# Kernel optimization log

Hardware: AMD Instinct MI355X
Metric: run time of the kernel (lower is better)

Reference implementation:

```python
import jax, jax.numpy as jnp
import numpy as np

HEADS = 4
DIM_HEAD = 32
SCALE = 10.0
EPS = 1e-12

def l2norm_axis1(t):
    # Faithful to source: default axis=1 -> normalize over the SEQUENCE axis of [B,N,h,d]
    denom = jnp.clip(jnp.linalg.norm(t, ord=2, axis=1, keepdims=True), EPS)
    return t / denom

def setup_inputs() -> dict:
    key = jax.random.key(0)
    k1, k2, k3 = jax.random.split(key, 3)
    B, N, C = 4, 4096, 128
    dim = HEADS * DIM_HEAD  # 128
    x = jax.random.normal(k1, (B, N, C), dtype=jnp.float32)
    W_qkv = jax.random.normal(k2, (C, 3 * dim), dtype=jnp.float32) * (1.0 / np.sqrt(C))
    W_out = jax.random.normal(k3, (dim, C), dtype=jnp.float32) * (1.0 / np.sqrt(dim))
    b_out = jnp.zeros((C,), dtype=jnp.float32)
    return {"x": x, "W_qkv": W_qkv, "W_out": W_out, "b_out": b_out}

def reference(x, W_qkv, W_out, b_out):
    B, N, C = x.shape
    # 1x1 conv == per-token linear
    qkv = jnp.einsum('bnc,ce->bne', x, W_qkv)  # [B,N,3*dim]
    q, k, v = jnp.split(qkv, 3, axis=-1)
    # [B,N,h,d]
    q = q.reshape(B, N, HEADS, DIM_HEAD)
    k = k.reshape(B, N, HEADS, DIM_HEAD)
    v = v.reshape(B, N, HEADS, DIM_HEAD)
    q = l2norm_axis1(q)
    k = l2norm_axis1(k)
    sim = jnp.einsum('bihd,bjhd->bhij', q, k) * SCALE  # [B,h,N,N]
    attn = jax.nn.softmax(sim, axis=-1)
    out = jnp.einsum('bhij,bjhd->bhid', attn, v)  # [B,h,N,d]
    out = out.transpose(0, 2, 1, 3).reshape(B, N, HEADS * DIM_HEAD)  # [B,N,dim]
    return jnp.einsum('bne,ec->bnc', out, W_out) + b_out
```

## Files before the change

### kernel.cpp

```cpp
#include <hip/hip_runtime.h>

typedef short s16x8 __attribute__((ext_vector_type(8)));
typedef short s16x4 __attribute__((ext_vector_type(4)));
typedef float f32x4 __attribute__((ext_vector_type(4)));
typedef float f4 __attribute__((ext_vector_type(4)));
typedef unsigned short u16x4 __attribute__((ext_vector_type(4)));

#define CEXP 14.426950408889634074f

__device__ __forceinline__ unsigned short f2bf(float f) {
    union { float f; unsigned int i; } v; v.f = f;
    unsigned int x = v.i;
    return (unsigned short)((x + 0x7fffu + ((x >> 16) & 1u)) >> 16);
}
__device__ __forceinline__ float bf2f(unsigned short u) {
    union { unsigned int i; float f; } v; v.i = ((unsigned int)u) << 16; return v.f;
}

__device__ __forceinline__ f32x4 mfma16x16x16_bf16(s16x4 a, s16x4 b, f32x4 c) {
#if __has_builtin(__builtin_amdgcn_mfma_f32_16x16x16bf16_1k)
    return __builtin_amdgcn_mfma_f32_16x16x16bf16_1k(a, b, c, 0, 0, 0);
#else
    f32x4 d = c;
    asm("v_mfma_f32_16x16x16_bf16 %0, %1, %2, %0" : "+v"(d) : "v"(a), "v"(b));
    return d;
#endif
}

__device__ __forceinline__ s16x4 pk_bf16x4(float p0, float p1, float p2, float p3) {
#if __has_builtin(__builtin_amdgcn_cvt_pk_bf16_f32)
    typedef __bf16 bf16x2 __attribute__((ext_vector_type(2)));
    union { struct { bf16x2 a, b; } h; s16x4 s; } r;
    r.h.a = __builtin_amdgcn_cvt_pk_bf16_f32(p0, p1);
    r.h.b = __builtin_amdgcn_cvt_pk_bf16_f32(p2, p3);
    return r.s;
#else
    unsigned u0 = __float_as_uint(p0) + 0x8000u;
    unsigned u1 = __float_as_uint(p1) + 0x8000u;
    unsigned u2 = __float_as_uint(p2) + 0x8000u;
    unsigned u3 = __float_as_uint(p3) + 0x8000u;
    union { uint2 u; s16x4 s; } pb;
    pb.u.x = __builtin_amdgcn_perm(u1, u0, 0x07060302u);
    pb.u.y = __builtin_amdgcn_perm(u3, u2, 0x07060302u);
    return pb.s;
#endif
}

__device__ __forceinline__ u16x4 pk4(f4 v) {
    u16x4 r = { f2bf(v[0]), f2bf(v[1]), f2bf(v[2]), f2bf(v[3]) };
    return r;
}

__global__ __launch_bounds__(256) void k_prep(
    const float* __restrict__ Wqkv, const float* __restrict__ Wout,
    unsigned short* __restrict__ Wt, unsigned short* __restrict__ WoT,
    float* __restrict__ sumsqp)
{
    const int blk = blockIdx.x, tid = threadIdx.x;
    if (blk < 192) {
        int e = blk * 256 + tid;
        int n = e >> 7, k = e & 127;
        Wt[e] = f2bf(Wqkv[k * 384 + n]);
    } else if (blk < 256) {
        int e = (blk - 192) * 256 + tid;
        int n = e >> 7, k = e & 127;
        WoT[e] = f2bf(Wout[k * 128 + n]);
    } else {
        sumsqp[(blk - 256) * 256 + tid] = 0.f;
    }
}

__global__ __launch_bounds__(256, 4) void k_qkv(
    const float* __restrict__ x, const unsigned short* __restrict__ Wt,
    unsigned short* __restrict__ Qb, unsigned short* __restrict__ Kb,
    unsigned short* __restrict__ Vt, float* __restrict__ sumsqp)
{
    __shared__ float red[4][64];
    const int tid = threadIdx.x;
    const int wl = tid >> 6, lane = tid & 63;
    const int qd = lane >> 4, nn = lane & 15;
    const int n0 = blockIdx.y * 64;
    const int tw0 = blockIdx.x * 64 + wl * 16;

    const float* apf = x + (size_t)(tw0 + nn) * 128 + qd * 8;
    const unsigned short* bp = Wt + (size_t)(n0 + nn) * 128 + qd * 8;
    s16x8 af[4], bfr[16];
#pragma unroll
    for (int ks = 0; ks < 4; ++ks) {
        f4 a0 = *(const f4*)(apf + ks * 32);
        f4 a1 = *(const f4*)(apf + ks * 32 + 4);
        union { struct { s16x4 lo, hi; } h; s16x8 v; } u;
        u.h.lo = pk_bf16x4(a0[0], a0[1], a0[2], a0[3]);
        u.h.hi = pk_bf16x4(a1[0], a1[1], a1[2], a1[3]);
        af[ks] = u.v;
    }
#pragma unroll
    for (int nb = 0; nb < 4; ++nb)
#pragma unroll
        for (int ks = 0; ks < 4; ++ks)
            bfr[nb * 4 + ks] = *(const s16x8*)(bp + (size_t)nb * 2048 + ks * 32);

    f32x4 acc[4];
#pragma unroll
    for (int nb = 0; nb < 4; ++nb) acc[nb] = (f32x4){0.f, 0.f, 0.f, 0.f};

    const int cb = n0 >> 7;
    const int b = tw0 >> 12;
    const int tl0 = tw0 & 4095;

    if (cb < 2) {
#pragma unroll
        for (int ks = 0; ks < 4; ++ks)
#pragma unroll
            for (int nb = 0; nb < 4; ++nb)
                acc[nb] = __builtin_amdgcn_mfma_f32_16x16x32_bf16(bfr[nb * 4 + ks], af[ks], acc[nb], 0, 0, 0);
        unsigned short* dst = (cb == 0) ? Qb : Kb;
        const int tok = tl0 + nn;
#pragma unroll
        for (int nb = 0; nb < 4; ++nb) {
            const int dim = (n0 & 127) + nb * 16 + qd * 4;
            const int h = dim >> 5, d0 = dim & 31;
            *(u16x4*)&dst[(size_t)((b * 4 + h) * 4096 + tok) * 32 + d0] = pk4(acc[nb]);
            f32x4 ss;
#pragma unroll
            for (int r = 0; r < 4; ++r) ss[r] = acc[nb][r] * acc[nb][r];
#pragma unroll
            for (int m = 1; m < 16; m <<= 1) {
#pragma unroll
                for (int r = 0; r < 4; ++r) ss[r] += __shfl_xor(ss[r], m);
            }
            if (nn == 0)
                *(f4*)&red[wl][nb * 16 + qd * 4] = ss;
        }
        __syncthreads();
        if (tid < 64) {
            float s = red[0][tid] + red[1][tid] + red[2][tid] + red[3][tid];
            const int g = (cb << 9) + (b << 7) + (n0 & 127) + tid;
            atomicAdd(&sumsqp[((blockIdx.x & 7) << 10) + g], s);
        }
    } else {
#pragma unroll
        for (int ks = 0; ks < 4; ++ks)
#pragma unroll
            for (int nb = 0; nb < 4; ++nb)
                acc[nb] = __builtin_amdgcn_mfma_f32_16x16x32_bf16(af[ks], bfr[nb * 4 + ks], acc[nb], 0, 0, 0);
#pragma unroll
        for (int nb = 0; nb < 4; ++nb) {
            const int dim = (n0 & 127) + nb * 16 + nn;
            const int h = dim >> 5, d = dim & 31;
            *(u16x4*)&Vt[(size_t)((b * 4 + h) * 32 + d) * 4096 + tl0 + qd * 4] = pk4(acc[nb]);
        }
    }
}

__global__ __launch_bounds__(512, 2) void k_attn(
    const unsigned short* __restrict__ Qb, const unsigned short* __restrict__ Kb,
    const unsigned short* __restrict__ Vt, const float* __restrict__ sumsqp,
    unsigned short* __restrict__ Ogb)
{
    __shared__ char smem[32768];
    const int tid  = threadIdx.x;
    const int wv   = tid >> 6, lane = tid & 63;
    const int wl   = wv & 3, half = wv >> 2;
    const int qd   = lane >> 4, nn = lane & 15;
    const int bh   = blockIdx.x;
    const int ib   = blockIdx.y * 128 + wl * 32;
    const unsigned short* Qbh = Qb + (size_t)bh * 4096 * 32;
    const unsigned short* Kbh = Kb + (size_t)bh * 4096 * 32;
    const unsigned short* Vbh = Vt + (size_t)bh * 32 * 4096;

    float rj[8];
    {
        const int gq = bh * 32 + qd * 8;
#pragma unroll
        for (int j = 0; j < 8; ++j) {
            float sq = 0.f, sk = 0.f;
#pragma unroll
            for (int c = 0; c < 8; ++c) {
                sq += sumsqp[c * 1024 + gq + j];
                sk += sumsqp[c * 1024 + 512 + gq + j];
            }
            rj[j] = fminf(__builtin_amdgcn_rsqf(sq), 1e12f)
                  * fminf(__builtin_amdgcn_rsqf(sk), 1e12f) * CEXP;
        }
    }

    s16x8 q0r = *(const s16x8*)(Qbh + (ib + nn) * 32 + qd * 8);
    s16x8 q1r = *(const s16x8*)(Qbh + (ib + 16 + nn) * 32 + qd * 8);
    s16x8 qf0, qf1;
#pragma unroll
    for (int j = 0; j < 8; ++j) {
        qf0[j] = (short)f2bf(bf2f((unsigned short)q0r[j]) * rj[j]);
        qf1[j] = (short)f2bf(bf2f((unsigned short)q1r[j]) * rj[j]);
    }

    f32x4 o00 = {0.f,0.f,0.f,0.f}, o01 = {0.f,0.f,0.f,0.f};
    f32x4 o10 = {0.f,0.f,0.f,0.f}, o11 = {0.f,0.f,0.f,0.f};
    const f32x4 zro = {0.f,0.f,0.f,0.f};
    float lpa = 0.f, lpb = 0.f;

    const int KB0 = half * 8192;
    const int VB0 = 16384 + half * 8192;
    const int jb0 = half * 2048;

    const unsigned short* ksrc = Kbh + (size_t)(jb0 + wl * 16 + nn) * 32 + qd * 8;
    const unsigned short* vsrc = Vbh + (size_t)(nn + 16 * (wl >> 1)) * 4096
                               + jb0 + ((wl & 1) * 2 + (qd >> 1)) * 16 + (qd & 1) * 8;
    char* kdst = smem + KB0 + wl * 1024 + lane * 16;
    char* vdst = smem + VB0 + wl * 1024 + lane * 16;

    {
        uint4 gk = *(const uint4*)ksrc;
        uint4 gv = *(const uint4*)vsrc;
        ksrc += 2048; vsrc += 64;
        *(uint4*)kdst = gk;
        *(uint4*)vdst = gv;
    }

    const int vro = (qd >> 1) * 256 + nn * 16 + (qd & 1) * 8;

    for (int jt = 0; jt < 32; ++jt) {
        uint4 ngk = *(const uint4*)ksrc;
        uint4 ngv = *(const uint4*)vsrc;
        ksrc += 2048; vsrc += 64;

        __syncthreads();
        const char* kcur = smem + KB0 + (jt & 1) * 4096;
        const char* vcur = smem + VB0 + (jt & 1) * 4096;
#pragma unroll
        for (int js = 0; js < 4; ++js) {
            s16x8 kf = *(const s16x8*)(kcur + js * 1024 + lane * 16);
            f32x4 sa = __builtin_amdgcn_mfma_f32_16x16x32_bf16(kf, qf0, zro, 0, 0, 0);
            f32x4 sb = __builtin_amdgcn_mfma_f32_16x16x32_bf16(kf, qf1, zro, 0, 0, 0);
            float a0 = __builtin_amdgcn_exp2f(sa[0]);
            float a1 = __builtin_amdgcn_exp2f(sa[1]);
            float a2 = __builtin_amdgcn_exp2f(sa[2]);
            float a3 = __builtin_amdgcn_exp2f(sa[3]);
            float b0 = __builtin_amdgcn_exp2f(sb[0]);
            float b1 = __builtin_amdgcn_exp2f(sb[1]);
            float b2 = __builtin_amdgcn_exp2f(sb[2]);
            float b3 = __builtin_amdgcn_exp2f(sb[3]);
            lpa += (a0 + a1) + (a2 + a3);
            lpb += (b0 + b1) + (b2 + b3);
            s16x4 pa = pk_bf16x4(a0, a1, a2, a3);
            s16x4 pb = pk_bf16x4(b0, b1, b2, b3);
            s16x4 va = *(const s16x4*)(vcur + js * 512 + vro);
            s16x4 vb = *(const s16x4*)(vcur + 2048 + js * 512 + vro);
            o00 = mfma16x16x16_bf16(va, pa, o00);
            o01 = mfma16x16x16_bf16(vb, pa, o01);
            o10 = mfma16x16x16_bf16(va, pb, o10);
            o11 = mfma16x16x16_bf16(vb, pb, o11);
        }
        const int nxt4k = ((jt + 1) & 1) * 4096;
        *(uint4*)(kdst + nxt4k) = ngk;
        *(uint4*)(vdst + nxt4k) = ngv;
    }

    lpa += __shfl_xor(lpa, 16);
    lpa += __shfl_xor(lpa, 32);
    lpb += __shfl_xor(lpb, 16);
    lpb += __shfl_xor(lpb, 32);
    __syncthreads();
    float* Ob = (float*)smem;
    float* Lb = (float*)(smem + 16384);
    if (half) {
        float* d0 = Ob + ((wl * 2 + 0) * 64 + lane) * 8;
        *(f4*)d0 = o00; *(f4*)(d0 + 4) = o01;
        float* d1 = Ob + ((wl * 2 + 1) * 64 + lane) * 8;
        *(f4*)d1 = o10; *(f4*)(d1 + 4) = o11;
        Lb[(wl * 2 + 0) * 64 + lane] = lpa;
        Lb[(wl * 2 + 1) * 64 + lane] = lpb;
    }
    __syncthreads();
    if (!half) {
        const int bb = bh >> 2, hh = bh & 3;
        float* s0 = Ob + ((wl * 2 + 0) * 64 + lane) * 8;
        float rla = 1.f / (lpa + Lb[(wl * 2 + 0) * 64 + lane]);
        f4 m00 = (o00 + *(const f4*)s0) * rla;
        f4 m01 = (o01 + *(const f4*)(s0 + 4)) * rla;
        float* s1 = Ob + ((wl * 2 + 1) * 64 + lane) * 8;
        float rlb = 1.f / (lpb + Lb[(wl * 2 + 1) * 64 + lane]);
        f4 m10 = (o10 + *(const f4*)s1) * rlb;
        f4 m11 = (o11 + *(const f4*)(s1 + 4)) * rlb;
        unsigned short* dst0 = Ogb + (size_t)(bb * 4096 + blockIdx.y * 128 + wl * 32 + nn) * 128
                             + hh * 32 + qd * 4;
        *(u16x4*)dst0 = pk4(m00);
        *(u16x4*)(dst0 + 16) = pk4(m01);
        unsigned short* dst1 = dst0 + (size_t)16 * 128;
        *(u16x4*)dst1 = pk4(m10);
        *(u16x4*)(dst1 + 16) = pk4(m11);
    }
}

__global__ __launch_bounds__(256, 4) void k_out(
    const unsigned short* __restrict__ Ogb, const unsigned short* __restrict__ WoT,
    const float* __restrict__ bout, float* __restrict__ out)
{
    const int tid = threadIdx.x;
    const int wl = tid >> 6, lane = tid & 63;
    const int qd = lane >> 4, nn = lane & 15;
    const int n0 = blockIdx.y * 64;
    const int tw0 = blockIdx.x * 64 + wl * 16;

    const unsigned short* ap = WoT + (size_t)(n0 + nn) * 128 + qd * 8;
    const unsigned short* bp = Ogb + (size_t)(tw0 + nn) * 128 + qd * 8;
    s16x8 bfr[4], afr[16];
#pragma unroll
    for (int ks = 0; ks < 4; ++ks) bfr[ks] = *(const s16x8*)(bp + ks * 32);
#pragma unroll
    for (int nb = 0; nb < 4; ++nb)
#pragma unroll
        for (int ks = 0; ks < 4; ++ks)
            afr[nb * 4 + ks] = *(const s16x8*)(ap + (size_t)nb * 2048 + ks * 32);

    f32x4 acc[4];
#pragma unroll
    for (int nb = 0; nb < 4; ++nb) acc[nb] = (f32x4){0.f, 0.f, 0.f, 0.f};
#pragma unroll
    for (int ks = 0; ks < 4; ++ks)
#pragma unroll
        for (int nb = 0; nb < 4; ++nb)
            acc[nb] = __builtin_amdgcn_mfma_f32_16x16x32_bf16(afr[nb * 4 + ks], bfr[ks], acc[nb], 0, 0, 0);

#pragma unroll
    for (int nb = 0; nb < 4; ++nb) {
        const int c = n0 + nb * 16 + qd * 4;
        f4 bv = *(const f4*)&bout[c];
        f4 r;
#pragma unroll
        for (int j = 0; j < 4; ++j) r[j] = acc[nb][j] + bv[j];
        *(f4*)&out[(size_t)(tw0 + nn) * 128 + c] = r;
    }
}

extern "C" void kernel_launch(void* const* d_in, const int* in_sizes, int n_in,
                              void* d_out, int out_size, void* d_ws, size_t ws_size,
                              hipStream_t stream)
{
    const float* x    = (const float*)d_in[0];
    const float* Wqkv = (const float*)d_in[1];
    const float* Wout = (const float*)d_in[2];
    const float* bout = (const float*)d_in[3];
    float* out = (float*)d_out;
    char* ws = (char*)d_ws;
    const size_t MB = 1024 * 1024;
    unsigned short* Qb  = (unsigned short*)(ws);
    unsigned short* Kb  = (unsigned short*)(ws + 4 * MB);
    unsigned short* Vt  = (unsigned short*)(ws + 8 * MB);
    unsigned short* Ogb = (unsigned short*)(ws + 12 * MB);
    unsigned short* Wt  = (unsigned short*)(ws + 16 * MB);
    unsigned short* WoT = (unsigned short*)(ws + 16 * MB + 112 * 1024);
    float*       sumsqp = (float*)(ws + 16 * MB + 160 * 1024);

    hipLaunchKernelGGL(k_prep, dim3(288), dim3(256), 0, stream, Wqkv, Wout, Wt, WoT, sumsqp);
    hipLaunchKernelGGL(k_qkv, dim3(256, 6), dim3(256), 0, stream, x, Wt, Qb, Kb, Vt, sumsqp);
    hipLaunchKernelGGL(k_attn, dim3(16, 32), dim3(512), 0, stream, Qb, Kb, Vt, sumsqp, Ogb);
    hipLaunchKernelGGL(k_out, dim3(256, 2), dim3(256), 0, stream, Ogb, WoT, bout, out);
}
```

Baseline: 148.9 us.

## Tile weight transpose in LDS, compute softmax row sums via MFMA, retune launch bounds

The weight prep kernel now transposes 64x64 tiles through shared memory, so both reads and writes are coalesced. It also shrinks the grid from 288 blocks to 48. In the attention kernel, the softmax denominator is now accumulated by an extra MFMA against a vector of ones instead of scalar adds and cross-lane shuffles, which moves VALU work onto the matrix unit. The denominator now sums the bf16-rounded probabilities. Launch-bound occupancy hints change for the qkv, attn and out kernels, which may alter register allocation and risk spills in attn at 4 blocks per SM.

Result: no change. 146.8 us (-1.4%).

```diff
diff --git a/kernel.cpp b/kernel.cpp
--- a/kernel.cpp
+++ b/kernel.cpp
@@ -56,21 +56,38 @@
     unsigned short* __restrict__ Wt, unsigned short* __restrict__ WoT,
     float* __restrict__ sumsqp)
 {
+    __shared__ float tile[64][65];
     const int blk = blockIdx.x, tid = threadIdx.x;
-    if (blk < 192) {
-        int e = blk * 256 + tid;
-        int n = e >> 7, k = e & 127;
-        Wt[e] = f2bf(Wqkv[k * 384 + n]);
-    } else if (blk < 256) {
-        int e = (blk - 192) * 256 + tid;
-        int n = e >> 7, k = e & 127;
-        WoT[e] = f2bf(Wout[k * 128 + n]);
+    if (blk >= 16) {
+        sumsqp[(blk - 16) * 256 + tid] = 0.f;
+        return;
+    }
+    const float* src;
+    unsigned short* dst;
+    int lds_src, k0, n0;
+    if (blk < 12) {
+        src = Wqkv; dst = Wt; lds_src = 384;
+        k0 = (blk & 1) * 64; n0 = (blk >> 1) * 64;
     } else {
-        sumsqp[(blk - 256) * 256 + tid] = 0.f;
-    }
-}
-
-__global__ __launch_bounds__(256, 4) void k_qkv(
+        int b = blk - 12;
+        src = Wout; dst = WoT; lds_src = 128;
+        k0 = (b & 1) * 64; n0 = (b >> 1) * 64;
+    }
+    const int c = tid & 63, r0 = tid >> 6;
+#pragma unroll
+    for (int i = 0; i < 16; ++i) {
+        int row = i * 4 + r0;
+        tile[row][c] = src[(size_t)(k0 + row) * lds_src + n0 + c];
+    }
+    __syncthreads();
+#pragma unroll
+    for (int i = 0; i < 16; ++i) {
+        int n = i * 4 + r0;
+        dst[(size_t)(n0 + n) * 128 + k0 + c] = f2bf(tile[c][n]);
+    }
+}
+
+__global__ __launch_bounds__(256, 2) void k_qkv(
     const float* __restrict__ x, const unsigned short* __restrict__ Wt,
     unsigned short* __restrict__ Qb, unsigned short* __restrict__ Kb,
     unsigned short* __restrict__ Vt, float* __restrict__ sumsqp)
@@ -153,7 +170,7 @@
     }
 }
 
-__global__ __launch_bounds__(512, 2) void k_attn(
+__global__ __launch_bounds__(512, 4) void k_attn(
     const unsigned short* __restrict__ Qb, const unsigned short* __restrict__ Kb,
     const unsigned short* __restrict__ Vt, const float* __restrict__ sumsqp,
     unsigned short* __restrict__ Ogb)
@@ -196,8 +213,9 @@
 
     f32x4 o00 = {0.f,0.f,0.f,0.f}, o01 = {0.f,0.f,0.f,0.f};
     f32x4 o10 = {0.f,0.f,0.f,0.f}, o11 = {0.f,0.f,0.f,0.f};
+    f32x4 la  = {0.f,0.f,0.f,0.f}, lb  = {0.f,0.f,0.f,0.f};
     const f32x4 zro = {0.f,0.f,0.f,0.f};
-    float lpa = 0.f, lpb = 0.f;
+    const s16x4 ones1 = { (short)0x3F80, (short)0x3F80, (short)0x3F80, (short)0x3F80 };
 
     const int KB0 = half * 8192;
     const int VB0 = 16384 + half * 8192;
@@ -240,10 +258,10 @@
             float b1 = __builtin_amdgcn_exp2f(sb[1]);
             float b2 = __builtin_amdgcn_exp2f(sb[2]);
             float b3 = __builtin_amdgcn_exp2f(sb[3]);
-            lpa += (a0 + a1) + (a2 + a3);
-            lpb += (b0 + b1) + (b2 + b3);
             s16x4 pa = pk_bf16x4(a0, a1, a2, a3);
             s16x4 pb = pk_bf16x4(b0, b1, b2, b3);
+            la = mfma16x16x16_bf16(ones1, pa, la);
+            lb = mfma16x16x16_bf16(ones1, pb, lb);
             s16x4 va = *(const s16x4*)(vcur + js * 512 + vro);
             s16x4 vb = *(const s16x4*)(vcur + 2048 + js * 512 + vro);
             o00 = mfma16x16x16_bf16(va, pa, o00);
@@ -256,10 +274,8 @@
         *(uint4*)(vdst + nxt4k) = ngv;
     }
 
-    lpa += __shfl_xor(lpa, 16);
-    lpa += __shfl_xor(lpa, 32);
-    lpb += __shfl_xor(lpb, 16);
-    lpb += __shfl_xor(lpb, 32);
+    const float lpa = la[0];
+    const float lpb = lb[0];
     __syncthreads();
     float* Ob = (float*)smem;
     float* Lb = (float*)(smem + 16384);
@@ -292,7 +308,7 @@
     }
 }
 
-__global__ __launch_bounds__(256, 4) void k_out(
+__global__ __launch_bounds__(256, 2) void k_out(
     const unsigned short* __restrict__ Ogb, const unsigned short* __restrict__ WoT,
     const float* __restrict__ bout, float* __restrict__ out)
 {
@@ -352,7 +368,7 @@
     unsigned short* WoT = (unsigned short*)(ws + 16 * MB + 112 * 1024);
     float*       sumsqp = (float*)(ws + 16 * MB + 160 * 1024);
 
-    hipLaunchKernelGGL(k_prep, dim3(288), dim3(256), 0, stream, Wqkv, Wout, Wt, WoT, sumsqp);
+    hipLaunchKernelGGL(k_prep, dim3(48), dim3(256), 0, stream, Wqkv, Wout, Wt, WoT, sumsqp);
     hipLaunchKernelGGL(k_qkv, dim3(256, 6), dim3(256), 0, stream, x, Wt, Qb, Kb, Vt, sumsqp);
     hipLaunchKernelGGL(k_attn, dim3(16, 32), dim3(512), 0, stream, Qb, Kb, Vt, sumsqp, Ogb);
     hipLaunchKernelGGL(k_out, dim3(256, 2), dim3(256), 0, stream, Ogb, WoT, bout, out);
```
